# Optimization experiments

Measured on AMD Instinct MI355X. Metric: run time of the kernel, lower is better.

Reference implementation:

```python
import jax, jax.numpy as jnp
import numpy as np

THRESHOLD = 0.9
EPS = 1e-12


def setup_inputs() -> dict:
    key = jax.random.key(0)
    ks = jax.random.split(key, 7)
    B, D_in, H1, H2, D_out = 8192, 256, 512, 256, 64
    # torch Linear default init ~ U(-1/sqrt(fan_in), 1/sqrt(fan_in)); randn scaled is fine as a stand-in
    def lin(k, out_f, in_f):
        return jax.random.normal(k, (out_f, in_f), dtype=jnp.float32) / np.sqrt(in_f)
    return {
        "x": jax.random.normal(ks[0], (B, D_in), dtype=jnp.float32),
        "W1": lin(ks[1], H1, D_in),
        "b1": jax.random.normal(ks[2], (H1,), dtype=jnp.float32) * 0.01,
        "W2": lin(ks[3], H2, H1),
        "b2": jax.random.normal(ks[4], (H2,), dtype=jnp.float32) * 0.01,
        "W3": lin(ks[5], D_out, H2),
        "b3": jax.random.normal(ks[6], (D_out,), dtype=jnp.float32) * 0.01,
    }


def reference(x, W1, b1, W2, b2, W3, b3):
    # MLP: Linear -> Tanh -> Linear -> Tanh -> Linear (no tanh on last)
    h1 = jnp.tanh(x @ W1.T + b1)          # [B, 512]
    h2 = jnp.tanh(h1 @ W2.T + b2)         # [B, 256]
    out = h2 @ W3.T + b3                  # [B, 64]

    # Pairwise state fidelity: (normalized dot)^2, thresholded adjacency (diag excluded)
    norms = jnp.linalg.norm(out, axis=-1, keepdims=True)  # [B, 1]
    normed = out / (norms + EPS)
    fid = (normed @ normed.T) ** 2                         # [B, B]
    adj = (fid >= THRESHOLD).astype(out.dtype)
    B = out.shape[0]
    adj = adj * (1.0 - jnp.eye(B, dtype=out.dtype))        # no self-edges (i < j pairs only)

    return adj @ out                                       # [B, 64]
```

## Files before the change

### kernel.cpp

```cpp
#include <hip/hip_runtime.h>
#include <hip/hip_bf16.h>
#include <math.h>

#define B_ROWS 8192
#define D_IN   256
#define H1_DIM 512
#define H2_DIM 256
#define D_OUT  64
#define EPSF   1e-12f
#define THRESH 0.9f

typedef __attribute__((ext_vector_type(8))) short short8;
typedef __attribute__((ext_vector_type(4))) float f32x4;

__device__ inline void pack8(const float* __restrict__ src, short* __restrict__ dh,
                             short* __restrict__ dm, int t, int C, int lgq) {
  const int lane = t & 63;
  const int g = t >> 6;
  const int q = g & ((1 << lgq) - 1);
  const int I = g >> lgq;
  const int row = I * 16 + (lane & 15);
  const int k0 = q * 32 + ((lane >> 4) << 3);
  const float* p = src + (size_t)row * C + k0;
  float4 a = *(const float4*)p;
  float4 b = *(const float4*)(p + 4);
  float v[8] = {a.x, a.y, a.z, a.w, b.x, b.y, b.z, b.w};
  short h8[8], m8[8];
#pragma unroll
  for (int e = 0; e < 8; ++e) {
    __hip_bfloat16 h = __float2bfloat16(v[e]);
    float hf = __bfloat162float(h);
    __hip_bfloat16 m = __float2bfloat16(v[e] - hf);
    h8[e] = *(short*)&h;
    m8[e] = *(short*)&m;
  }
  *(short8*)(dh + (size_t)t * 8) = *(short8*)h8;
  *(short8*)(dm + (size_t)t * 8) = *(short8*)m8;
}

__global__ __launch_bounds__(256)
void pack_inputs(const float* __restrict__ x, const float* __restrict__ W1,
                 const float* __restrict__ W2, const float* __restrict__ W3,
                 short* xh, short* xm, short* w1h, short* w1m,
                 short* w2h, short* w2m, short* w3h, short* w3m) {
  const int b = blockIdx.x;
  const int tid = threadIdx.x;
  if (b < 1024)       pack8(x,  xh,  xm,  b * 256 + tid, 256, 3);
  else if (b < 1088)  pack8(W1, w1h, w1m, (b - 1024) * 256 + tid, 256, 3);
  else if (b < 1152)  pack8(W2, w2h, w2m, (b - 1088) * 256 + tid, 512, 4);
  else                pack8(W3, w3h, w3m, (b - 1152) * 256 + tid, 256, 3);
}

template<int KSTEPS, int JT, int MODE>
__global__ __launch_bounds__(256, 2)
void mfma_gemm(const short* __restrict__ pAh, const short* __restrict__ pAm,
               const short* __restrict__ pBh, const short* __restrict__ pBm,
               const float* __restrict__ bias, float* __restrict__ Cout,
               short* __restrict__ dh, short* __restrict__ dm, int N,
               float* __restrict__ rz) {
  constexpr int ITB = 4;
  constexpr int BTJ = 2 * JT;
  constexpr int NITEMS = 2 * ITB + 2 * BTJ;
  constexpr int PER_WAVE = NITEMS / 4;
  constexpr int WCOL = 16 * JT + 4;
  union SM {
    struct {
      short Ah[2][ITB * 512];
      short Am[2][ITB * 512];
      short Bh[2][BTJ * 512];
      short Bm[2][BTJ * 512];
    } st;
    float wbuf[4 * 32 * WCOL];
  };
  __shared__ __align__(16) SM sm;
  __shared__ float nsum[2][64];
  __shared__ float invn[64];

  const int tid = threadIdx.x;
  const int wave = tid >> 6, lane = tid & 63;
  const int wi = wave >> 1, wj = wave & 1;
  const int bIt0 = blockIdx.x * ITB;
  const int bJt0 = blockIdx.y * BTJ;

  if constexpr (MODE == 2) {
    float4* rz4 = (float4*)(rz + (size_t)blockIdx.x * 64 * 64);
#pragma unroll
    for (int u = 0; u < 4; ++u)
      rz4[u * 256 + tid] = make_float4(0.f, 0.f, 0.f, 0.f);
  }

  f32x4 acc[2][JT];
#pragma unroll
  for (int a = 0; a < 2; ++a)
#pragma unroll
    for (int b = 0; b < JT; ++b) acc[a][b] = (f32x4){0.f, 0.f, 0.f, 0.f};

  auto stage = [&](int q, int bf) {
#pragma unroll
    for (int u = 0; u < PER_WAVE; ++u) {
      const int item = wave * PER_WAVE + u;
      const short* src;
      short* dst;
      if (item < 2 * ITB) {
        const int t = item >> 1;
        const int m = item & 1;
        src = (m ? pAm : pAh) + ((size_t)(bIt0 + t) * KSTEPS + q) * 512;
        dst = (m ? sm.st.Am : sm.st.Ah)[bf] + t * 512;
      } else {
        const int e = item - 2 * ITB;
        const int t = e >> 1;
        const int m = e & 1;
        src = (m ? pBm : pBh) + ((size_t)(bJt0 + t) * KSTEPS + q) * 512;
        dst = (m ? sm.st.Bm : sm.st.Bh)[bf] + t * 512;
      }
      __builtin_amdgcn_global_load_lds(
          (const __attribute__((address_space(1))) void*)(src + lane * 8),
          (__attribute__((address_space(3))) void*)dst, 16, 0, 0);
    }
  };

  stage(0, 0);
  for (int q = 0; q < KSTEPS; ++q) {
    __syncthreads();
    if (q + 1 < KSTEPS) stage(q + 1, (q + 1) & 1);
    const int bf = q & 1;
    short8 Ah[2], Am[2];
#pragma unroll
    for (int it = 0; it < 2; ++it) {
      Ah[it] = *(const short8*)(sm.st.Ah[bf] + (wi * 2 + it) * 512 + lane * 8);
      Am[it] = *(const short8*)(sm.st.Am[bf] + (wi * 2 + it) * 512 + lane * 8);
    }
    short8 Bh[JT], Bm[JT];
#pragma unroll
    for (int jt = 0; jt < JT; ++jt) {
      Bh[jt] = *(const short8*)(sm.st.Bh[bf] + (wj * JT + jt) * 512 + lane * 8);
      Bm[jt] = *(const short8*)(sm.st.Bm[bf] + (wj * JT + jt) * 512 + lane * 8);
    }
#pragma unroll
    for (int it = 0; it < 2; ++it)
#pragma unroll
      for (int jt = 0; jt < JT; ++jt) {
        acc[it][jt] = __builtin_amdgcn_mfma_f32_16x16x32_bf16(Ah[it], Bh[jt], acc[it][jt], 0, 0, 0);
        acc[it][jt] = __builtin_amdgcn_mfma_f32_16x16x32_bf16(Ah[it], Bm[jt], acc[it][jt], 0, 0, 0);
        acc[it][jt] = __builtin_amdgcn_mfma_f32_16x16x32_bf16(Am[it], Bh[jt], acc[it][jt], 0, 0, 0);
      }
  }
  __syncthreads();

  float bv[JT];
#pragma unroll
  for (int jt = 0; jt < JT; ++jt)
    bv[jt] = bias[(bJt0 + wj * JT + jt) * 16 + (lane & 15)];

  if constexpr (MODE == 1) {
#pragma unroll
    for (int it = 0; it < 2; ++it)
#pragma unroll
      for (int jt = 0; jt < JT; ++jt)
#pragma unroll
        for (int r = 0; r < 4; ++r) {
          const float val = tanhf(acc[it][jt][r] + bv[jt]);
          const int row_l = it * 16 + (lane >> 4) * 4 + r;
          const int col_l = jt * 16 + (lane & 15);
          sm.wbuf[(wave * 32 + row_l) * WCOL + col_l] = val;
        }
    __syncthreads();
  } else {
#pragma unroll
    for (int it = 0; it < 2; ++it)
#pragma unroll
      for (int r = 0; r < 4; ++r) {
        float sq = 0.f;
        const int row_l = it * 16 + (lane >> 4) * 4 + r;
#pragma unroll
        for (int jt = 0; jt < JT; ++jt) {
          const float val = acc[it][jt][r] + bv[jt];
          const int col_l = jt * 16 + (lane & 15);
          sm.wbuf[(wave * 32 + row_l) * WCOL + col_l] = val;
          const int row = (bIt0 + wi * 2 + it) * 16 + (lane >> 4) * 4 + r;
          Cout[(size_t)row * N + wj * (16 * JT) + col_l] = val;
          sq = fmaf(val, val, sq);
        }
#pragma unroll
        for (int m = 1; m < 16; m <<= 1) sq += __shfl_xor(sq, m, 64);
        if ((lane & 15) == 0) nsum[wj][wi * 32 + row_l] = sq;
      }
    __syncthreads();
    if (tid < 64) invn[tid] = 1.0f / (sqrtf(nsum[0][tid] + nsum[1][tid]) + EPSF);
    __syncthreads();
  }

  constexpr int QLMAX = (JT >= 2) ? (JT / 2) : 1;
#pragma unroll
  for (int itl = 0; itl < 2; ++itl)
#pragma unroll
    for (int ql = 0; ql < QLMAX; ++ql) {
      const int row_l = itl * 16 + (lane & 15);
      const int kl = ql * 32 + ((lane >> 4) << 3);
      const float* wp = &sm.wbuf[(wave * 32 + row_l) * WCOL + kl];
      const float scale = (MODE == 2) ? invn[wi * 32 + row_l] : 1.0f;
      float4 a = *(const float4*)wp;
      float4 b = *(const float4*)(wp + 4);
      float v[8] = {a.x, a.y, a.z, a.w, b.x, b.y, b.z, b.w};
      short h8[8], m8[8];
#pragma unroll
      for (int e = 0; e < 8; ++e) {
        const float sv = v[e] * scale;
        __hip_bfloat16 h = __float2bfloat16(sv);
        float hf = __bfloat162float(h);
        __hip_bfloat16 m = __float2bfloat16(sv - hf);
        h8[e] = *(short*)&h;
        m8[e] = *(short*)&m;
      }
      const int ItG = bIt0 + wi * 2 + itl;
      const int qG = (((bJt0 + wj * JT) * 16) + ql * 32) >> 5;
      const size_t off = ((size_t)(ItG * (N >> 5) + qG) * 64 + lane) * 8;
      *(short8*)(dh + off) = *(short8*)h8;
      *(short8*)(dm + off) = *(short8*)m8;
    }
}

#define JSPLIT 8
#define CT 8
#define NCHUNK (B_ROWS / JSPLIT / 16 / CT)

__global__ __launch_bounds__(256, 2)
void gram_accum(const short* __restrict__ vph, const short* __restrict__ vpm,
                const float* __restrict__ out, float* __restrict__ res) {
  __shared__ __align__(16) short lh[2][CT * 1024];
  __shared__ __align__(16) short lm[2][CT * 1024];
  const int tid = threadIdx.x;
  const int wave = tid >> 6;
  const int lane = tid & 63;
  const int i0 = blockIdx.x * 128;
  const int jbase = blockIdx.y * (B_ROWS / JSPLIT);

  short8 Ah[8][2], Am[8][2];
#pragma unroll
  for (int it = 0; it < 8; ++it) {
    const int It = (i0 >> 4) + it;
#pragma unroll
    for (int q = 0; q < 2; ++q) {
      Ah[it][q] = *(const short8*)(vph + (size_t)It * 1024 + q * 512 + lane * 8);
      Am[it][q] = *(const short8*)(vpm + (size_t)It * 1024 + q * 512 + lane * 8);
    }
  }

  auto stage = [&](int c, int bf) {
    const size_t base = ((size_t)(jbase >> 4) + c * CT) * 1024;
#pragma unroll
    for (int u = 0; u < 8; ++u) {
      const int item = wave * 8 + u;
      const short* src;
      short* dst;
      if (item < 16) { src = vph + base + item * 512; dst = lh[bf] + item * 512; }
      else           { src = vpm + base + (item - 16) * 512; dst = lm[bf] + (item - 16) * 512; }
      __builtin_amdgcn_global_load_lds(
          (const __attribute__((address_space(1))) void*)(src + lane * 8),
          (__attribute__((address_space(3))) void*)dst, 16, 0, 0);
    }
  };

  stage(0, 0);
  for (int c = 0; c < NCHUNK; ++c) {
    __syncthreads();
    if (c + 1 < NCHUNK) stage(c + 1, (c + 1) & 1);
    const int bf = c & 1;
#pragma unroll
    for (int t = 0; t < 2; ++t) {
      const int jt = wave * 2 + t;
      const int j0 = jbase + (c * CT + jt) * 16;
      short8 Bh0 = *(const short8*)(lh[bf] + jt * 1024 + lane * 8);
      short8 Bh1 = *(const short8*)(lh[bf] + jt * 1024 + 512 + lane * 8);
      short8 Bm0 = *(const short8*)(lm[bf] + jt * 1024 + lane * 8);
      short8 Bm1 = *(const short8*)(lm[bf] + jt * 1024 + 512 + lane * 8);
      f32x4 g[8];
#pragma unroll
      for (int it = 0; it < 8; ++it) g[it] = (f32x4){0.f, 0.f, 0.f, 0.f};
#pragma unroll
      for (int it = 0; it < 8; ++it) g[it] = __builtin_amdgcn_mfma_f32_16x16x32_bf16(Ah[it][0], Bh0, g[it], 0, 0, 0);
#pragma unroll
      for (int it = 0; it < 8; ++it) g[it] = __builtin_amdgcn_mfma_f32_16x16x32_bf16(Ah[it][1], Bh1, g[it], 0, 0, 0);
#pragma unroll
      for (int it = 0; it < 8; ++it) g[it] = __builtin_amdgcn_mfma_f32_16x16x32_bf16(Ah[it][0], Bm0, g[it], 0, 0, 0);
#pragma unroll
      for (int it = 0; it < 8; ++it) g[it] = __builtin_amdgcn_mfma_f32_16x16x32_bf16(Am[it][0], Bh0, g[it], 0, 0, 0);
#pragma unroll
      for (int it = 0; it < 8; ++it) g[it] = __builtin_amdgcn_mfma_f32_16x16x32_bf16(Ah[it][1], Bm1, g[it], 0, 0, 0);
#pragma unroll
      for (int it = 0; it < 8; ++it) g[it] = __builtin_amdgcn_mfma_f32_16x16x32_bf16(Am[it][1], Bh1, g[it], 0, 0, 0);
#pragma unroll
      for (int it = 0; it < 8; ++it) {
        const float m01 = fmaxf(g[it][0] * g[it][0], g[it][1] * g[it][1]);
        const float m23 = fmaxf(g[it][2] * g[it][2], g[it][3] * g[it][3]);
        if (fmaxf(m01, m23) >= THRESH) {
          const int j = j0 + (lane & 15);
          const float* __restrict__ oj = out + (size_t)j * D_OUT;
#pragma unroll
          for (int r = 0; r < 4; ++r) {
            if (g[it][r] * g[it][r] >= THRESH) {
              const int i = i0 + it * 16 + (lane >> 4) * 4 + r;
              if (i != j) {
                float* __restrict__ ri = res + (size_t)i * D_OUT;
                for (int k = 0; k < D_OUT; ++k) atomicAdd(&ri[k], oj[k]);
              }
            }
          }
        }
      }
    }
  }
}

#define MB (1024 * 1024)

extern "C" void kernel_launch(void* const* d_in, const int* in_sizes, int n_in,
                              void* d_out, int out_size, void* d_ws, size_t ws_size,
                              hipStream_t stream) {
  const float* x  = (const float*)d_in[0];
  const float* W1 = (const float*)d_in[1];
  const float* b1 = (const float*)d_in[2];
  const float* W2 = (const float*)d_in[3];
  const float* b2 = (const float*)d_in[4];
  const float* W3 = (const float*)d_in[5];
  const float* b3 = (const float*)d_in[6];
  float* res = (float*)d_out;

  char* ws = (char*)d_ws;
  short* xh  = (short*)(ws + 0 * MB);
  short* xm  = (short*)(ws + 4 * MB);
  short* h2h = (short*)(ws + 0 * MB);
  short* h2m = (short*)(ws + 4 * MB);
  short* h1h = (short*)(ws + 8 * MB);
  short* h1m = (short*)(ws + 16 * MB);
  float* out = (float*)(ws + 8 * MB);
  short* vph = (short*)(ws + 11 * MB);
  short* vpm = (short*)(ws + 12 * MB);
  short* w1h = (short*)(ws + 24 * MB);
  short* w1m = (short*)(ws + 24 * MB + 256 * 1024);
  short* w2h = (short*)(ws + 24 * MB + 512 * 1024);
  short* w2m = (short*)(ws + 24 * MB + 768 * 1024);
  short* w3h = (short*)(ws + 25 * MB);
  short* w3m = (short*)(ws + 25 * MB + 32 * 1024);

  pack_inputs<<<1160, 256, 0, stream>>>(x, W1, W2, W3, xh, xm, w1h, w1m, w2h, w2m, w3h, w3m);
  mfma_gemm<8, 4, 1><<<dim3(128, 4), 256, 0, stream>>>(
      xh, xm, w1h, w1m, b1, nullptr, h1h, h1m, H1_DIM, nullptr);
  mfma_gemm<16, 2, 1><<<dim3(128, 4), 256, 0, stream>>>(
      h1h, h1m, w2h, w2m, b2, nullptr, h2h, h2m, H2_DIM, nullptr);
  mfma_gemm<8, 2, 2><<<dim3(128, 1), 256, 0, stream>>>(
      h2h, h2m, w3h, w3m, b3, out, vph, vpm, D_OUT, res);
  gram_accum<<<dim3(B_ROWS / 128, JSPLIT), 256, 0, stream>>>(vph, vpm, out, res);
}
```

Baseline: 129.9 us.

## Exploit Gram symmetry with triangular tiling and skip low-order MFMA outside threshold band

The Gram accumulation now visits only upper-triangular 128x128 tile pairs, decoding each block index into a tile pair with a sqrt formula. Each qualifying i<j pair adds both contributions via atomics, which roughly halves the MFMA work. The bf16 hi/lo split corrections run only when some fidelity in a wave falls near the threshold band, so most tiles use a single bf16 product. This changes correctness margins, since a product outside the band is classified from hi-only precision, and it adds a second atomic stream per edge. The A lo fragments are now read from LDS on demand instead of being held in registers.

```diff
diff --git a/kernel.cpp b/kernel.cpp
--- a/kernel.cpp
+++ b/kernel.cpp
@@ -9,6 +9,8 @@
 #define D_OUT  64
 #define EPSF   1e-12f
 #define THRESH 0.9f
+#define BAND_LO 0.89f
+#define BAND_HI 0.91f
 
 typedef __attribute__((ext_vector_type(8))) short short8;
 typedef __attribute__((ext_vector_type(4))) float f32x4;
@@ -220,89 +222,105 @@
     }
 }
 
-#define JSPLIT 8
-#define CT 8
-#define NCHUNK (B_ROWS / JSPLIT / 16 / CT)
-
 __global__ __launch_bounds__(256, 2)
 void gram_accum(const short* __restrict__ vph, const short* __restrict__ vpm,
                 const float* __restrict__ out, float* __restrict__ res) {
-  __shared__ __align__(16) short lh[2][CT * 1024];
-  __shared__ __align__(16) short lm[2][CT * 1024];
+  __shared__ __align__(16) short lAh[8 * 1024];
+  __shared__ __align__(16) short lAm[8 * 1024];
   const int tid = threadIdx.x;
-  const int wave = tid >> 6;
-  const int lane = tid & 63;
-  const int i0 = blockIdx.x * 128;
-  const int jbase = blockIdx.y * (B_ROWS / JSPLIT);
-
-  short8 Ah[8][2], Am[8][2];
-#pragma unroll
-  for (int it = 0; it < 8; ++it) {
-    const int It = (i0 >> 4) + it;
-#pragma unroll
-    for (int q = 0; q < 2; ++q) {
-      Ah[it][q] = *(const short8*)(vph + (size_t)It * 1024 + q * 512 + lane * 8);
-      Am[it][q] = *(const short8*)(vpm + (size_t)It * 1024 + q * 512 + lane * 8);
-    }
-  }
-
-  auto stage = [&](int c, int bf) {
-    const size_t base = ((size_t)(jbase >> 4) + c * CT) * 1024;
+  const int wave = tid >> 6, lane = tid & 63;
+
+  const int t = blockIdx.x;
+  int I = (int)((129.0f - sqrtf(16641.0f - 8.0f * (float)t)) * 0.5f);
+  if (I < 0) I = 0;
+  while (64 * (I + 1) - ((I + 1) * I) / 2 <= t) ++I;
+  while (64 * I - (I * (I - 1)) / 2 > t) --I;
+  const int Jc = I + (t - (64 * I - (I * (I - 1)) / 2));
+  const int i0 = I * 128;
+  const int j0c = Jc * 128;
+
+  {
+    const size_t base = (size_t)I * 8192;
 #pragma unroll
     for (int u = 0; u < 8; ++u) {
       const int item = wave * 8 + u;
       const short* src;
       short* dst;
-      if (item < 16) { src = vph + base + item * 512; dst = lh[bf] + item * 512; }
-      else           { src = vpm + base + (item - 16) * 512; dst = lm[bf] + (item - 16) * 512; }
+      if (item < 16) { src = vph + base + item * 512; dst = lAh + item * 512; }
+      else           { src = vpm + base + (item - 16) * 512; dst = lAm + (item - 16) * 512; }
       __builtin_amdgcn_global_load_lds(
           (const __attribute__((address_space(1))) void*)(src + lane * 8),
           (__attribute__((address_space(3))) void*)dst, 16, 0, 0);
     }
-  };
-
-  stage(0, 0);
-  for (int c = 0; c < NCHUNK; ++c) {
-    __syncthreads();
-    if (c + 1 < NCHUNK) stage(c + 1, (c + 1) & 1);
-    const int bf = c & 1;
-#pragma unroll
-    for (int t = 0; t < 2; ++t) {
-      const int jt = wave * 2 + t;
-      const int j0 = jbase + (c * CT + jt) * 16;
-      short8 Bh0 = *(const short8*)(lh[bf] + jt * 1024 + lane * 8);
-      short8 Bh1 = *(const short8*)(lh[bf] + jt * 1024 + 512 + lane * 8);
-      short8 Bm0 = *(const short8*)(lm[bf] + jt * 1024 + lane * 8);
-      short8 Bm1 = *(const short8*)(lm[bf] + jt * 1024 + 512 + lane * 8);
-      f32x4 g[8];
-#pragma unroll
-      for (int it = 0; it < 8; ++it) g[it] = (f32x4){0.f, 0.f, 0.f, 0.f};
-#pragma unroll
-      for (int it = 0; it < 8; ++it) g[it] = __builtin_amdgcn_mfma_f32_16x16x32_bf16(Ah[it][0], Bh0, g[it], 0, 0, 0);
-#pragma unroll
-      for (int it = 0; it < 8; ++it) g[it] = __builtin_amdgcn_mfma_f32_16x16x32_bf16(Ah[it][1], Bh1, g[it], 0, 0, 0);
+  }
+  __syncthreads();
+
+  short8 Ah[8][2];
+#pragma unroll
+  for (int it = 0; it < 8; ++it)
+#pragma unroll
+    for (int q = 0; q < 2; ++q)
+      Ah[it][q] = *(const short8*)(lAh + it * 1024 + q * 512 + lane * 8);
+
+#pragma unroll
+  for (int tt = 0; tt < 2; ++tt) {
+    const int jt = wave * 2 + tt;
+    const int j0 = j0c + jt * 16;
+    const short* jb_h = vph + (size_t)(j0 >> 4) * 1024;
+    short8 Bh0 = *(const short8*)(jb_h + lane * 8);
+    short8 Bh1 = *(const short8*)(jb_h + 512 + lane * 8);
+
+    f32x4 g[8];
+#pragma unroll
+    for (int it = 0; it < 8; ++it) g[it] = (f32x4){0.f, 0.f, 0.f, 0.f};
+#pragma unroll
+    for (int it = 0; it < 8; ++it) g[it] = __builtin_amdgcn_mfma_f32_16x16x32_bf16(Ah[it][0], Bh0, g[it], 0, 0, 0);
+#pragma unroll
+    for (int it = 0; it < 8; ++it) g[it] = __builtin_amdgcn_mfma_f32_16x16x32_bf16(Ah[it][1], Bh1, g[it], 0, 0, 0);
+
+    bool band = false;
+#pragma unroll
+    for (int it = 0; it < 8; ++it)
+#pragma unroll
+      for (int r = 0; r < 4; ++r) {
+        const float f = g[it][r] * g[it][r];
+        band = band || (f > BAND_LO && f < BAND_HI);
+      }
+    if (__any(band)) {
+      const short* jb_m = vpm + (size_t)(j0 >> 4) * 1024;
+      short8 Bm0 = *(const short8*)(jb_m + lane * 8);
+      short8 Bm1 = *(const short8*)(jb_m + 512 + lane * 8);
 #pragma unroll
       for (int it = 0; it < 8; ++it) g[it] = __builtin_amdgcn_mfma_f32_16x16x32_bf16(Ah[it][0], Bm0, g[it], 0, 0, 0);
 #pragma unroll
-      for (int it = 0; it < 8; ++it) g[it] = __builtin_amdgcn_mfma_f32_16x16x32_bf16(Am[it][0], Bh0, g[it], 0, 0, 0);
-#pragma unroll
       for (int it = 0; it < 8; ++it) g[it] = __builtin_amdgcn_mfma_f32_16x16x32_bf16(Ah[it][1], Bm1, g[it], 0, 0, 0);
 #pragma unroll
-      for (int it = 0; it < 8; ++it) g[it] = __builtin_amdgcn_mfma_f32_16x16x32_bf16(Am[it][1], Bh1, g[it], 0, 0, 0);
-#pragma unroll
       for (int it = 0; it < 8; ++it) {
-        const float m01 = fmaxf(g[it][0] * g[it][0], g[it][1] * g[it][1]);
-        const float m23 = fmaxf(g[it][2] * g[it][2], g[it][3] * g[it][3]);
-        if (fmaxf(m01, m23) >= THRESH) {
-          const int j = j0 + (lane & 15);
-          const float* __restrict__ oj = out + (size_t)j * D_OUT;
-#pragma unroll
-          for (int r = 0; r < 4; ++r) {
-            if (g[it][r] * g[it][r] >= THRESH) {
-              const int i = i0 + it * 16 + (lane >> 4) * 4 + r;
-              if (i != j) {
-                float* __restrict__ ri = res + (size_t)i * D_OUT;
-                for (int k = 0; k < D_OUT; ++k) atomicAdd(&ri[k], oj[k]);
+        short8 Am0 = *(const short8*)(lAm + it * 1024 + lane * 8);
+        short8 Am1 = *(const short8*)(lAm + it * 1024 + 512 + lane * 8);
+        g[it] = __builtin_amdgcn_mfma_f32_16x16x32_bf16(Am0, Bh0, g[it], 0, 0, 0);
+        g[it] = __builtin_amdgcn_mfma_f32_16x16x32_bf16(Am1, Bh1, g[it], 0, 0, 0);
+      }
+    }
+
+    const int j = j0 + (lane & 15);
+#pragma unroll
+    for (int it = 0; it < 8; ++it) {
+      const float m01 = fmaxf(g[it][0] * g[it][0], g[it][1] * g[it][1]);
+      const float m23 = fmaxf(g[it][2] * g[it][2], g[it][3] * g[it][3]);
+      if (fmaxf(m01, m23) >= THRESH) {
+        const float* __restrict__ oj = out + (size_t)j * D_OUT;
+#pragma unroll
+        for (int r = 0; r < 4; ++r) {
+          if (g[it][r] * g[it][r] >= THRESH) {
+            const int i = i0 + it * 16 + (lane >> 4) * 4 + r;
+            if (i < j) {
+              float* __restrict__ ri = res + (size_t)i * D_OUT;
+              float* __restrict__ rj = res + (size_t)j * D_OUT;
+              const float* __restrict__ oi = out + (size_t)i * D_OUT;
+              for (int k = 0; k < D_OUT; ++k) {
+                atomicAdd(&ri[k], oj[k]);
+                atomicAdd(&rj[k], oi[k]);
               }
             }
           }
@@ -350,5 +368,5 @@
       h1h, h1m, w2h, w2m, b2, nullptr, h2h, h2m, H2_DIM, nullptr);
   mfma_gemm<8, 2, 2><<<dim3(128, 1), 256, 0, stream>>>(
       h2h, h2m, w3h, w3m, b3, out, vph, vpm, D_OUT, res);
-  gram_accum<<<dim3(B_ROWS / 128, JSPLIT), 256, 0, stream>>>(vph, vpm, out, res);
-}
+  gram_accum<<<dim3(2080), 256, 0, stream>>>(vph, vpm, out, res);
+}
```

Measured after the change: 128.1 us. No clear change (-1.4%).
